# Performance work log

Measured on AMD Instinct MI355X. Metric: run time of the kernel, lower is better.

Reference implementation:

```python
import jax, jax.numpy as jnp
import numpy as np

N = 8192          # batch of labeled text embeddings
D = 256           # embedding dim
NUM_LABELS = 128  # distinct cluster labels


def setup_inputs() -> dict:
    key = jax.random.key(0)
    k1, k2 = jax.random.split(key)
    embeddings = jax.random.normal(k1, (N, D), dtype=jnp.float32)
    labels = jax.random.randint(k2, (N,), 0, NUM_LABELS, dtype=jnp.int64)
    logit_scale = jnp.array([20.0], dtype=jnp.float32)  # 1 / temperature, temperature=0.05
    return {"embeddings": embeddings, "labels": labels, "logit_scale": logit_scale}


def reference(embeddings, labels, logit_scale):
    # Equivalent reformulation of the per-group python loop:
    # for each label group g with >=2 members,
    #   contribution = (sum_{j!=k in g} exp(-s*sim_jk)) * (sum_{j in g, l not in g} exp(s*sim_jl))
    # loss = log(1 + sum_g contribution)
    s = logit_scale[0]
    eps = 1e-12  # matches torch F.normalize clamp
    e = embeddings / jnp.maximum(jnp.linalg.norm(embeddings, axis=1, keepdims=True), eps)
    S = (e @ e.T) * s                                   # [N, N] scaled cosine similarity
    n = labels.shape[0]
    same = labels[:, None] == labels[None, :]           # [N, N] same-label mask
    offdiag = ~jnp.eye(n, dtype=bool)
    pos_mask = same & offdiag                           # same label, j != k
    neg_mask = ~same                                    # different label
    # per-row partial sums (fused exp+mask+reduce under jit)
    a = jnp.sum(jnp.exp(-S) * pos_mask, axis=1)         # [N] positive-pair terms
    b = jnp.sum(jnp.exp(S) * neg_mask, axis=1)          # [N] negative-pair terms
    # aggregate per label group
    counts = jax.ops.segment_sum(jnp.ones((n,), dtype=jnp.float32), labels, num_segments=NUM_LABELS)
    A = jax.ops.segment_sum(a, labels, num_segments=NUM_LABELS)
    B = jax.ops.segment_sum(b, labels, num_segments=NUM_LABELS)
    valid = counts >= 2.0                               # groups with <2 members are skipped
    sum_value = 1.0 + jnp.sum(jnp.where(valid, A * B, 0.0))
    return jnp.log(sum_value)
```

## Files before the change

### kernel.cpp

```cpp
#include <hip/hip_runtime.h>
#include <hip/hip_bf16.h>
#include <math.h>


typedef __attribute__((ext_vector_type(2))) long l2;
typedef __attribute__((ext_vector_type(4))) float f32x4;

#define N_EMB 8192
#define D_EMB 256
#define NUM_LABELS 128
#define PAN 128
#define NPAN (N_EMB / PAN)
#define NTRI (NPAN * (NPAN + 1) / 2)

template <int CTRL>
__device__ __forceinline__ float dpp_add(float x) {
    int y = __builtin_amdgcn_update_dpp(0, __builtin_bit_cast(int, x),
                                        CTRL, 0xF, 0xF, false);
    return x + __builtin_bit_cast(float, y);
}
__device__ __forceinline__ float red16(float x) {
    x = dpp_add<0xB1>(x);
    x = dpp_add<0x4E>(x);
    x = dpp_add<0x124>(x);
    x = dpp_add<0x128>(x);
    return x;
}

__device__ __forceinline__ unsigned packbf(float a, float b) {
    unsigned ua = __builtin_bit_cast(unsigned, a);
    unsigned ub = __builtin_bit_cast(unsigned, b);
    ua += 0x7FFFu + ((ua >> 16) & 1u);
    ub += 0x7FFFu + ((ub >> 16) & 1u);
    return (ua >> 16) | (ub & 0xFFFF0000u);
}

__global__ __launch_bounds__(256) void normalize_kernel(const float* __restrict__ emb,
                                                        char* __restrict__ e8) {
    const int wid = threadIdx.x >> 6, lane = threadIdx.x & 63;
    const int row = blockIdx.x * 4 + wid;
    const f32x4 x = *(const f32x4*)(emb + (size_t)row * D_EMB + lane * 4);
    float ss = x[0]*x[0] + x[1]*x[1] + x[2]*x[2] + x[3]*x[3];
    #pragma unroll
    for (int off = 32; off >= 1; off >>= 1) ss += __shfl_xor(ss, off);
    const float r = 1.0f / fmaxf(sqrtf(ss), 1e-12f);
    int v = __builtin_amdgcn_cvt_pk_fp8_f32(x[0] * r, x[1] * r, 0, false);
    v = __builtin_amdgcn_cvt_pk_fp8_f32(x[2] * r, x[3] * r, v, true);
    const int u    = lane >> 4;
    const int half = (lane >> 3) & 1;
    const int lp   = ((lane >> 1) & 3) * 16 + (row & 15);
    const int j0   = (lane & 1) * 4;
    char* dst = e8 + ((size_t)(row >> 4) * 4 + u) * 1024 + lp * 16 + half * 8 + j0;
    *(unsigned*)dst = (unsigned)v;
}

#define LOADF(dst, voff, sb, OFFSTR) \
    asm volatile("global_load_dwordx4 %0, %1, %2 offset:" OFFSTR \
                 : "=v"(dst) : "v"(voff), "s"(sb))

#define ISSUE(PA_, PB_, OFFSTR) \
    LOADF(PA_[0], voA[0], sbA, OFFSTR); LOADF(PA_[1], voA[1], sbA, OFFSTR); \
    LOADF(PA_[2], voA[2], sbA, OFFSTR); LOADF(PA_[3], voA[3], sbA, OFFSTR); \
    LOADF(PB_[0], voB[0], sbB, OFFSTR); LOADF(PB_[1], voB[1], sbB, OFFSTR); \
    LOADF(PB_[2], voB[2], sbB, OFFSTR); LOADF(PB_[3], voB[3], sbB, OFFSTR)

#define WAITV(NSTR) \
    asm volatile("s_waitcnt vmcnt(" NSTR ")" ::: "memory"); \
    __builtin_amdgcn_sched_barrier(0)

#define MF8(a, b, c) __builtin_amdgcn_mfma_f32_16x16x32_fp8_fp8(a, b, c, 0, 0, 0)

#define MROW(PA_, PB_, mi, H) \
    acc[mi][0] = MF8(PA_[mi][H], PB_[0][H], acc[mi][0]); \
    acc[mi][1] = MF8(PA_[mi][H], PB_[1][H], acc[mi][1]); \
    acc[mi][2] = MF8(PA_[mi][H], PB_[2][H], acc[mi][2]); \
    acc[mi][3] = MF8(PA_[mi][H], PB_[3][H], acc[mi][3]);

#define MFMA32(PA_, PB_) \
    __builtin_amdgcn_s_setprio(1); \
    MROW(PA_, PB_, 0, 0) MROW(PA_, PB_, 1, 0) MROW(PA_, PB_, 2, 0) MROW(PA_, PB_, 3, 0) \
    MROW(PA_, PB_, 0, 1) MROW(PA_, PB_, 1, 1) MROW(PA_, PB_, 2, 1) MROW(PA_, PB_, 3, 1) \
    __builtin_amdgcn_s_setprio(0)

__global__ __launch_bounds__(256, 3) void cosent_main(const char* __restrict__ e8,
                                                      const int* __restrict__ labels,
                                                      const float* __restrict__ scale,
                                                      unsigned* __restrict__ wsAB) {
    __shared__ float rowsc[2][PAN][2];
    __shared__ float colsc[2][PAN][2];
    __shared__ int labR[PAN], labC[PAN];

    const int bid = blockIdx.x;
    const int swz = (bid & 7) * 260 + (bid >> 3);
    int rem = swz, by = 0;
    while (rem >= NPAN - by) { rem -= NPAN - by; ++by; }
    const int bx = by + rem;
    const bool diag = (bx == by);
    const int rowBase = by * PAN, colBase = bx * PAN;

    const int tid = threadIdx.x, lane = tid & 63, wid = tid >> 6;
    const int wm = wid >> 1, wn = wid & 1;
    const int rr = lane & 15, kh = lane >> 4;

    if (tid < PAN) labR[tid] = labels[rowBase + tid];
    else           labC[tid - PAN] = labels[colBase + tid - PAN];
    __syncthreads();

    const int laneB = lane * 16;
    int voA[4], voB[4];
    #pragma unroll
    for (int i = 0; i < 4; ++i) {
        voA[i] = (wm * 4 + i) * 4096 + laneB;
        voB[i] = (wn * 4 + i) * 4096 + laneB;
    }
    const char* sbA = e8 + (size_t)rowBase * 256;
    const char* sbB = e8 + (size_t)colBase * 256;

    f32x4 acc[4][4];
    #pragma unroll
    for (int i = 0; i < 4; ++i)
        #pragma unroll
        for (int j = 0; j < 4; ++j) acc[i][j] = (f32x4){0.f, 0.f, 0.f, 0.f};

    l2 pA[4], pB[4], qA[4], qB[4];

    ISSUE(pA, pB, "0");
    ISSUE(qA, qB, "1024"); WAITV("8"); MFMA32(pA, pB);
    ISSUE(pA, pB, "2048"); WAITV("8"); MFMA32(qA, qB);
    ISSUE(qA, qB, "3072"); WAITV("8"); MFMA32(pA, pB);
    WAITV("0"); MFMA32(qA, qB);

    const float s = *scale;
    int lc[4];
    #pragma unroll
    for (int ni = 0; ni < 4; ++ni) lc[ni] = labC[wn * 64 + ni * 16 + rr];
    float colA[4] = {0.f, 0.f, 0.f, 0.f}, colB[4] = {0.f, 0.f, 0.f, 0.f};

    #pragma unroll
    for (int mi = 0; mi < 4; ++mi) {
        #pragma unroll
        for (int r = 0; r < 4; ++r) {
            const int rowL = wm * 64 + mi * 16 + kh * 4 + r;
            const int lr = labR[rowL];
            float asum = 0.f, bsum = 0.f;
            #pragma unroll
            for (int ni = 0; ni < 4; ++ni) {
                const int colL = wn * 64 + ni * 16 + rr;
                const float val = acc[mi][ni][r] * s;
                const bool pos = (lr == lc[ni]);
                float ex = __expf(pos ? -val : val);
                if (diag && rowL == colL) ex = 0.f;
                if (pos) { asum += ex; colA[ni] += ex; }
                else     { bsum += ex; colB[ni] += ex; }
            }
            asum = red16(asum);
            bsum = red16(bsum);
            if (rr == 0) { rowsc[wn][rowL][0] = asum; rowsc[wn][rowL][1] = bsum; }
        }
    }

    if (!diag) {
        #pragma unroll
        for (int ni = 0; ni < 4; ++ni) {
            float a = colA[ni], b = colB[ni];
            a += __shfl_xor(a, 16); a += __shfl_xor(a, 32);
            b += __shfl_xor(b, 16); b += __shfl_xor(b, 32);
            if (lane < 16) {
                colsc[wm][wn * 64 + ni * 16 + lane][0] = a;
                colsc[wm][wn * 64 + ni * 16 + lane][1] = b;
            }
        }
    }
    __syncthreads();

    if (tid < PAN) {
        const float ra = rowsc[0][tid][0] + rowsc[1][tid][0];
        const float rb = rowsc[0][tid][1] + rowsc[1][tid][1];
        wsAB[(size_t)bx * N_EMB + rowBase + tid] = packbf(ra, rb);
        if (!diag) {
            const float ca = colsc[0][tid][0] + colsc[1][tid][0];
            const float cb = colsc[0][tid][1] + colsc[1][tid][1];
            wsAB[(size_t)by * N_EMB + colBase + tid] = packbf(ca, cb);
        }
    }
}

__global__ __launch_bounds__(256) void reduce_rows(const unsigned* __restrict__ wsAB,
                                                   const int* __restrict__ labels,
                                                   float* __restrict__ part) {
    __shared__ float A[NUM_LABELS], B[NUM_LABELS];
    __shared__ int C[NUM_LABELS];
    const int tid = threadIdx.x;
    if (tid < NUM_LABELS) { A[tid] = 0.f; B[tid] = 0.f; C[tid] = 0; }
    __syncthreads();
    const int row = blockIdx.x * 256 + tid;
    float a = 0.f, b = 0.f;
    #pragma unroll
    for (int p = 0; p < NPAN; ++p) {
        const unsigned u = wsAB[(size_t)p * N_EMB + row];
        a += __builtin_bit_cast(float, u << 16);
        b += __builtin_bit_cast(float, u & 0xFFFF0000u);
    }
    const int l = labels[row];
    atomicAdd(&A[l], a);
    atomicAdd(&B[l], b);
    atomicAdd(&C[l], 1);
    __syncthreads();
    if (tid < NUM_LABELS) {
        float* p = part + ((size_t)blockIdx.x * NUM_LABELS + tid) * 3;
        p[0] = A[tid]; p[1] = B[tid]; p[2] = (float)C[tid];
    }
}

__global__ __launch_bounds__(128) void finalize_kernel(const float* __restrict__ part,
                                                       float* __restrict__ out) {
    const int tid = threadIdx.x;
    float A = 0.f, B = 0.f, c = 0.f;
    #pragma unroll
    for (int blk = 0; blk < 32; ++blk) {
        const float* p = part + ((size_t)blk * NUM_LABELS + tid) * 3;
        A += p[0]; B += p[1]; c += p[2];
    }
    float v = (c >= 2.f) ? A * B : 0.f;
    #pragma unroll
    for (int off = 32; off >= 1; off >>= 1) v += __shfl_xor(v, off);
    __shared__ float w2[2];
    if ((tid & 63) == 0) w2[tid >> 6] = v;
    __syncthreads();
    if (tid == 0) out[0] = logf(1.0f + w2[0] + w2[1]);
}

extern "C" void kernel_launch(void* const* d_in, const int* in_sizes, int n_in,
                              void* d_out, int out_size, void* d_ws, size_t ws_size,
                              hipStream_t stream) {
    const float* emb    = (const float*)d_in[0];
    const int*   labels = (const int*)d_in[1];
    const float* scale  = (const float*)d_in[2];
    float* out = (float*)d_out;

    char*     e8   = (char*)d_ws;
    unsigned* wsAB = (unsigned*)((char*)d_ws + (size_t)N_EMB * D_EMB);
    float*    part = (float*)((char*)wsAB + (size_t)NPAN * N_EMB * sizeof(unsigned));

    normalize_kernel<<<N_EMB / 4, 256, 0, stream>>>(emb, e8);
    cosent_main<<<NTRI, 256, 0, stream>>>(e8, labels, scale, wsAB);
    reduce_rows<<<N_EMB / 256, 256, 0, stream>>>(wsAB, labels, part);
    finalize_kernel<<<1, 128, 0, stream>>>(part, out);
}
```

Before: 47.14 us.

## Fold per-label aggregation into main kernel via LDS bins and global atomic slots

The main tile kernel now bins its row and column partial sums by label in shared memory. It then atomically adds them into one of 128 global slot arrays, which replaces the bf16-packed per-panel workspace and the separate reduce_rows kernel. The slots are zeroed inside the normalize kernel, and the finalize kernel now counts labels itself and sums the slots. Other changes: a closed-form sqrt tile-index decode replaces the loop, exp is done as a raw v_exp_f32 with log2e folded into the scale, and the first __syncthreads is deferred until after the MFMA loads. This removes one launch and a large workspace write and read, at the cost of global atomic contention and nondeterministic float summation order.

Measured after the change: 52.61 us. 11.6% more time.

```diff
diff --git a/kernel.cpp b/kernel.cpp
--- a/kernel.cpp
+++ b/kernel.cpp
@@ -12,6 +12,7 @@
 #define PAN 128
 #define NPAN (N_EMB / PAN)
 #define NTRI (NPAN * (NPAN + 1) / 2)
+#define NSLOT 128
 
 template <int CTRL>
 __device__ __forceinline__ float dpp_add(float x) {
@@ -27,16 +28,15 @@
     return x;
 }
 
-__device__ __forceinline__ unsigned packbf(float a, float b) {
-    unsigned ua = __builtin_bit_cast(unsigned, a);
-    unsigned ub = __builtin_bit_cast(unsigned, b);
-    ua += 0x7FFFu + ((ua >> 16) & 1u);
-    ub += 0x7FFFu + ((ub >> 16) & 1u);
-    return (ua >> 16) | (ub & 0xFFFF0000u);
+__device__ __forceinline__ float exp2hw(float x) {
+    float r;
+    asm("v_exp_f32 %0, %1" : "=v"(r) : "v"(x));
+    return r;
 }
 
 __global__ __launch_bounds__(256) void normalize_kernel(const float* __restrict__ emb,
-                                                        char* __restrict__ e8) {
+                                                        char* __restrict__ e8,
+                                                        float* __restrict__ slots) {
     const int wid = threadIdx.x >> 6, lane = threadIdx.x & 63;
     const int row = blockIdx.x * 4 + wid;
     const f32x4 x = *(const f32x4*)(emb + (size_t)row * D_EMB + lane * 4);
@@ -52,6 +52,7 @@
     const int j0   = (lane & 1) * 4;
     char* dst = e8 + ((size_t)(row >> 4) * 4 + u) * 1024 + lp * 16 + half * 8 + j0;
     *(unsigned*)dst = (unsigned)v;
+    if (blockIdx.x < NSLOT) slots[blockIdx.x * 256 + threadIdx.x] = 0.f;
 }
 
 #define LOADF(dst, voff, sb, OFFSTR) \
@@ -85,16 +86,19 @@
 __global__ __launch_bounds__(256, 3) void cosent_main(const char* __restrict__ e8,
                                                       const int* __restrict__ labels,
                                                       const float* __restrict__ scale,
-                                                      unsigned* __restrict__ wsAB) {
+                                                      float* __restrict__ slots) {
     __shared__ float rowsc[2][PAN][2];
     __shared__ float colsc[2][PAN][2];
+    __shared__ float binA[NUM_LABELS], binB[NUM_LABELS];
     __shared__ int labR[PAN], labC[PAN];
 
     const int bid = blockIdx.x;
     const int swz = (bid & 7) * 260 + (bid >> 3);
-    int rem = swz, by = 0;
-    while (rem >= NPAN - by) { rem -= NPAN - by; ++by; }
-    const int bx = by + rem;
+    int by = (int)((129.0f - sqrtf(16641.0f - 8.0f * (float)swz)) * 0.5f);
+    by = by < 0 ? 0 : (by > 63 ? 63 : by);
+    while (by < 63 && (by + 1) * (129 - (by + 1)) / 2 <= swz) ++by;
+    while (by > 0 && by * (129 - by) / 2 > swz) --by;
+    const int bx = by + (swz - by * (129 - by) / 2);
     const bool diag = (bx == by);
     const int rowBase = by * PAN, colBase = bx * PAN;
 
@@ -102,9 +106,8 @@
     const int wm = wid >> 1, wn = wid & 1;
     const int rr = lane & 15, kh = lane >> 4;
 
-    if (tid < PAN) labR[tid] = labels[rowBase + tid];
-    else           labC[tid - PAN] = labels[colBase + tid - PAN];
-    __syncthreads();
+    if (tid < PAN) { labR[tid] = labels[rowBase + tid]; binA[tid] = 0.f; binB[tid] = 0.f; }
+    else           { labC[tid - PAN] = labels[colBase + tid - PAN]; }
 
     const int laneB = lane * 16;
     int voA[4], voB[4];
@@ -130,7 +133,9 @@
     ISSUE(qA, qB, "3072"); WAITV("8"); MFMA32(pA, pB);
     WAITV("0"); MFMA32(qA, qB);
 
-    const float s = *scale;
+    __syncthreads();
+
+    const float s2 = *scale * 1.44269504088896f;
     int lc[4];
     #pragma unroll
     for (int ni = 0; ni < 4; ++ni) lc[ni] = labC[wn * 64 + ni * 16 + rr];
@@ -146,9 +151,9 @@
             #pragma unroll
             for (int ni = 0; ni < 4; ++ni) {
                 const int colL = wn * 64 + ni * 16 + rr;
-                const float val = acc[mi][ni][r] * s;
+                const float val = acc[mi][ni][r] * s2;
                 const bool pos = (lr == lc[ni]);
-                float ex = __expf(pos ? -val : val);
+                float ex = exp2hw(pos ? -val : val);
                 if (diag && rowL == colL) ex = 0.f;
                 if (pos) { asum += ex; colA[ni] += ex; }
                 else     { bsum += ex; colB[ni] += ex; }
@@ -176,58 +181,50 @@
     if (tid < PAN) {
         const float ra = rowsc[0][tid][0] + rowsc[1][tid][0];
         const float rb = rowsc[0][tid][1] + rowsc[1][tid][1];
-        wsAB[(size_t)bx * N_EMB + rowBase + tid] = packbf(ra, rb);
+        atomicAdd(&binA[labR[tid]], ra);
+        atomicAdd(&binB[labR[tid]], rb);
         if (!diag) {
             const float ca = colsc[0][tid][0] + colsc[1][tid][0];
             const float cb = colsc[0][tid][1] + colsc[1][tid][1];
-            wsAB[(size_t)by * N_EMB + colBase + tid] = packbf(ca, cb);
-        }
-    }
-}
-
-__global__ __launch_bounds__(256) void reduce_rows(const unsigned* __restrict__ wsAB,
-                                                   const int* __restrict__ labels,
-                                                   float* __restrict__ part) {
-    __shared__ float A[NUM_LABELS], B[NUM_LABELS];
-    __shared__ int C[NUM_LABELS];
+            atomicAdd(&binA[labC[tid]], ca);
+            atomicAdd(&binB[labC[tid]], cb);
+        }
+    }
+    __syncthreads();
+
+    if (tid < NUM_LABELS) {
+        float* slot = slots + (size_t)(bid & (NSLOT - 1)) * (NUM_LABELS * 2);
+        const float a = binA[tid], b = binB[tid];
+        if (a != 0.f) atomicAdd(&slot[tid * 2 + 0], a);
+        if (b != 0.f) atomicAdd(&slot[tid * 2 + 1], b);
+    }
+}
+
+__global__ __launch_bounds__(256) void finalize_kernel(const float* __restrict__ slots,
+                                                       const int* __restrict__ labels,
+                                                       float* __restrict__ out) {
+    __shared__ int cnt[NUM_LABELS];
+    __shared__ float w2[4];
     const int tid = threadIdx.x;
-    if (tid < NUM_LABELS) { A[tid] = 0.f; B[tid] = 0.f; C[tid] = 0; }
-    __syncthreads();
-    const int row = blockIdx.x * 256 + tid;
-    float a = 0.f, b = 0.f;
-    #pragma unroll
-    for (int p = 0; p < NPAN; ++p) {
-        const unsigned u = wsAB[(size_t)p * N_EMB + row];
-        a += __builtin_bit_cast(float, u << 16);
-        b += __builtin_bit_cast(float, u & 0xFFFF0000u);
-    }
-    const int l = labels[row];
-    atomicAdd(&A[l], a);
-    atomicAdd(&B[l], b);
-    atomicAdd(&C[l], 1);
-    __syncthreads();
+    if (tid < NUM_LABELS) cnt[tid] = 0;
+    __syncthreads();
+    for (int i = tid; i < N_EMB; i += 256) atomicAdd(&cnt[labels[i]], 1);
+    __syncthreads();
+
+    float A = 0.f, B = 0.f;
     if (tid < NUM_LABELS) {
-        float* p = part + ((size_t)blockIdx.x * NUM_LABELS + tid) * 3;
-        p[0] = A[tid]; p[1] = B[tid]; p[2] = (float)C[tid];
-    }
-}
-
-__global__ __launch_bounds__(128) void finalize_kernel(const float* __restrict__ part,
-                                                       float* __restrict__ out) {
-    const int tid = threadIdx.x;
-    float A = 0.f, B = 0.f, c = 0.f;
-    #pragma unroll
-    for (int blk = 0; blk < 32; ++blk) {
-        const float* p = part + ((size_t)blk * NUM_LABELS + tid) * 3;
-        A += p[0]; B += p[1]; c += p[2];
-    }
-    float v = (c >= 2.f) ? A * B : 0.f;
+        #pragma unroll 8
+        for (int s = 0; s < NSLOT; ++s) {
+            const float* p = slots + (size_t)s * (NUM_LABELS * 2) + tid * 2;
+            A += p[0]; B += p[1];
+        }
+    }
+    float v = (tid < NUM_LABELS && cnt[tid] >= 2) ? A * B : 0.f;
     #pragma unroll
     for (int off = 32; off >= 1; off >>= 1) v += __shfl_xor(v, off);
-    __shared__ float w2[2];
     if ((tid & 63) == 0) w2[tid >> 6] = v;
     __syncthreads();
-    if (tid == 0) out[0] = logf(1.0f + w2[0] + w2[1]);
+    if (tid == 0) out[0] = logf(1.0f + w2[0] + w2[1] + w2[2] + w2[3]);
 }
 
 extern "C" void kernel_launch(void* const* d_in, const int* in_sizes, int n_in,
@@ -238,12 +235,10 @@
     const float* scale  = (const float*)d_in[2];
     float* out = (float*)d_out;
 
-    char*     e8   = (char*)d_ws;
-    unsigned* wsAB = (unsigned*)((char*)d_ws + (size_t)N_EMB * D_EMB);
-    float*    part = (float*)((char*)wsAB + (size_t)NPAN * N_EMB * sizeof(unsigned));
-
-    normalize_kernel<<<N_EMB / 4, 256, 0, stream>>>(emb, e8);
-    cosent_main<<<NTRI, 256, 0, stream>>>(e8, labels, scale, wsAB);
-    reduce_rows<<<N_EMB / 256, 256, 0, stream>>>(wsAB, labels, part);
-    finalize_kernel<<<1, 128, 0, stream>>>(part, out);
-}
+    char*  e8    = (char*)d_ws;
+    float* slots = (float*)((char*)d_ws + (size_t)N_EMB * D_EMB);
+
+    normalize_kernel<<<N_EMB / 4, 256, 0, stream>>>(emb, e8, slots);
+    cosent_main<<<NTRI, 256, 0, stream>>>(e8, labels, scale, slots);
+    finalize_kernel<<<1, 256, 0, stream>>>(slots, labels, out);
+}
```
